# Kernel tuning notes

Measured on AMD Instinct MI355X. Metric: run time of the kernel, lower is better.

Reference implementation:

```python
import jax, jax.numpy as jnp
import numpy as np
from jax.scipy.special import logsumexp

EPS = 0.1
MAX_ITER = 10
THRESH = 0.1


def setup_inputs() -> dict:
    key = jax.random.key(0)
    k1, k2 = jax.random.split(key)
    N, P, D = 16, 1024, 64
    y = jax.random.normal(k1, (N, P, D), dtype=jnp.float32)
    x = jax.random.normal(k2, (N, P, D), dtype=jnp.float32)
    return {"y": y, "x": x}


def reference(y, x):
    # Cost matrix |x_i - y_j|^2 summed over feature dim: (N, P1, P2)
    C = jnp.sum(jnp.abs(x[:, :, None, :] - y[:, None, :, :]) ** 2, axis=-1)
    N, P1, P2 = C.shape
    mu = jnp.full((N, P1), 1.0 / P1, dtype=C.dtype)
    nu = jnp.full((N, P2), 1.0 / P2, dtype=C.dtype)

    def M(u, v):
        # (-C + u_i + v_j) / eps
        return (-C + u[:, :, None] + v[:, None, :]) / EPS

    def body(carry, _):
        u, v, done = carry
        u_new = EPS * (jnp.log(mu + 1e-8) - logsumexp(M(u, v), axis=-1)) + u
        v_new = EPS * (jnp.log(nu + 1e-8) - logsumexp(M(u_new, v), axis=-2)) + v
        err = jnp.abs(u_new - u).sum(-1).mean()
        # emulate torch's early break: freeze updates once converged
        u2 = jnp.where(done, u, u_new)
        v2 = jnp.where(done, v, v_new)
        done2 = done | (err < THRESH)
        return (u2, v2, done2), None

    u0 = jnp.zeros_like(mu)
    v0 = jnp.zeros_like(nu)
    (u, v, _), _ = jax.lax.scan(body, (u0, v0, jnp.array(False)), None, length=MAX_ITER)
    pi = jnp.exp(M(u, v))  # transport plan (N, P1, P2)
    return pi
```

## Files before the change

### kernel.cpp

```cpp
#include <hip/hip_runtime.h>
#include <math.h>

#define NB 16
#define PP 1024
#define DD 64
#define MAX_ITER 10
#define RCH 16
#define NCH (PP / RCH)
#define NBLK (NB * NCH)

constexpr float EPSV    = 0.1f;
constexpr float INV_EPS = 10.0f;
constexpr float LOG2E   = 1.44269504088896340736f;
constexpr float LOG_MU  = -6.93146156597137f;
constexpr float THRESHV = 0.1f;

__global__ __launch_bounds__(256) void compute_c(
    const float* __restrict__ x, const float* __restrict__ y,
    float* __restrict__ Cs)
{
  const int bid = blockIdx.x;
  const int n   = bid >> 8;
  const int ib  = (bid >> 4) & 15;
  const int jb  = bid & 15;

  __shared__ float xs[64][68];
  __shared__ float ys[64][68];

  const float* xb = x + ((size_t)n * PP + ib * 64) * DD;
  const float* yb = y + ((size_t)n * PP + jb * 64) * DD;

  for (int t = threadIdx.x; t < 64 * 16; t += 256) {
    int r = t >> 4, d4 = (t & 15) * 4;
    float4 v = *(const float4*)(xb + r * DD + d4);
    xs[r][d4] = v.x; xs[r][d4 + 1] = v.y; xs[r][d4 + 2] = v.z; xs[r][d4 + 3] = v.w;
  }
  for (int t = threadIdx.x; t < 64 * 16; t += 256) {
    int r = t >> 4, d4 = (t & 15) * 4;
    float4 v = *(const float4*)(yb + (size_t)r * DD + d4);
    ys[r][d4] = v.x; ys[r][d4 + 1] = v.y; ys[r][d4 + 2] = v.z; ys[r][d4 + 3] = v.w;
  }
  __syncthreads();

  const int tx = threadIdx.x & 15;
  const int ty = threadIdx.x >> 4;
  const int i0 = ty * 4;

  float acc[4][4] = {};
  for (int d0 = 0; d0 < 64; d0 += 4) {
    float4 xv[4], yv[4];
    #pragma unroll
    for (int ii = 0; ii < 4; ++ii) xv[ii] = *(const float4*)&xs[i0 + ii][d0];
    #pragma unroll
    for (int jj = 0; jj < 4; ++jj) yv[jj] = *(const float4*)&ys[tx + 16 * jj][d0];
    #pragma unroll
    for (int ii = 0; ii < 4; ++ii) {
      #pragma unroll
      for (int jj = 0; jj < 4; ++jj) {
        float d;
        d = xv[ii].x - yv[jj].x; acc[ii][jj] = fmaf(d, d, acc[ii][jj]);
        d = xv[ii].y - yv[jj].y; acc[ii][jj] = fmaf(d, d, acc[ii][jj]);
        d = xv[ii].z - yv[jj].z; acc[ii][jj] = fmaf(d, d, acc[ii][jj]);
        d = xv[ii].w - yv[jj].w; acc[ii][jj] = fmaf(d, d, acc[ii][jj]);
      }
    }
  }

  float* outb = Cs + ((size_t)n * PP + ib * 64) * PP + jb * 64;
  #pragma unroll
  for (int ii = 0; ii < 4; ++ii)
    #pragma unroll
    for (int jj = 0; jj < 4; ++jj)
      outb[(size_t)(i0 + ii) * PP + tx + 16 * jj] = acc[ii][jj] * INV_EPS;
}

__global__ __launch_bounds__(256, 4) void iter_fused(
    const float* __restrict__ Cs, float* __restrict__ aG, const float* __restrict__ bG,
    float* __restrict__ pm, float* __restrict__ ps, float* __restrict__ errBlk,
    const int* __restrict__ doneFlags, int it)
{
  if (it > 0 && doneFlags[it - 1]) return;

  const int n   = blockIdx.x >> 6;
  const int rc  = blockIdx.x & (NCH - 1);
  const int tid = threadIdx.x;

  __shared__ float bb[PP];
  __shared__ float aArr[RCH];
  __shared__ float dsum[RCH];

  if (it == 0) {
    *(float4*)&bb[tid * 4] = make_float4(0.f, 0.f, 0.f, 0.f);
  } else {
    *(float4*)&bb[tid * 4] = *(const float4*)(bG + n * PP + tid * 4);
  }
  __syncthreads();

  const int r0  = tid >> 4;
  const int k   = tid & 15;
  const int row = n * PP + rc * RCH + r0;
  const float* crow = Cs + (size_t)row * PP + 4 * k;

  float4 tv[16];
  #pragma unroll
  for (int j = 0; j < 16; ++j) {
    float4 c4 = *(const float4*)(crow + 64 * j);
    float4 b4 = *(const float4*)&bb[4 * k + 64 * j];
    tv[j] = make_float4(b4.x - c4.x, b4.y - c4.y, b4.z - c4.z, b4.w - c4.w);
  }
  float m = -INFINITY;
  #pragma unroll
  for (int j = 0; j < 16; ++j)
    m = fmaxf(m, fmaxf(fmaxf(tv[j].x, tv[j].y), fmaxf(tv[j].z, tv[j].w)));
  #pragma unroll
  for (int mask = 8; mask; mask >>= 1) m = fmaxf(m, __shfl_xor(m, mask));

  float s = 0.f;
  #pragma unroll
  for (int j = 0; j < 16; ++j) {
    s += exp2f((tv[j].x - m) * LOG2E) + exp2f((tv[j].y - m) * LOG2E)
       + exp2f((tv[j].z - m) * LOG2E) + exp2f((tv[j].w - m) * LOG2E);
  }
  #pragma unroll
  for (int mask = 8; mask; mask >>= 1) s += __shfl_xor(s, mask);

  if (k == 0) {
    float aOld = (it == 0) ? 0.f : aG[row];
    float an = LOG_MU - (m + logf(s));
    aG[row]  = an;
    aArr[r0] = an;
    dsum[r0] = fabsf(an - aOld);
  }
  __syncthreads();
  if (tid == 0) {
    float e = 0.f;
    #pragma unroll
    for (int r = 0; r < RCH; ++r) e += dsum[r];
    errBlk[blockIdx.x] = e;
  }

  const int c0 = tid * 4;
  const float* cb = Cs + ((size_t)(n * PP + rc * RCH)) * PP + c0;

  float m0 = -INFINITY, m1 = -INFINITY, m2 = -INFINITY, m3 = -INFINITY;
  #pragma unroll
  for (int r = 0; r < RCH; ++r) {
    float ar = aArr[r];
    float4 c4 = *(const float4*)(cb + (size_t)r * PP);
    m0 = fmaxf(m0, ar - c4.x);
    m1 = fmaxf(m1, ar - c4.y);
    m2 = fmaxf(m2, ar - c4.z);
    m3 = fmaxf(m3, ar - c4.w);
  }
  float s0 = 0.f, s1 = 0.f, s2 = 0.f, s3 = 0.f;
  #pragma unroll
  for (int r = 0; r < RCH; ++r) {
    float ar = aArr[r];
    float4 c4 = *(const float4*)(cb + (size_t)r * PP);
    s0 += exp2f((ar - c4.x - m0) * LOG2E);
    s1 += exp2f((ar - c4.y - m1) * LOG2E);
    s2 += exp2f((ar - c4.z - m2) * LOG2E);
    s3 += exp2f((ar - c4.w - m3) * LOG2E);
  }
  size_t off = ((size_t)(n * NCH + rc)) * PP + c0;
  *(float4*)(pm + off) = make_float4(m0, m1, m2, m3);
  *(float4*)(ps + off) = make_float4(s0, s1, s2, s3);
}

__global__ __launch_bounds__(256) void v_combine(
    const float* __restrict__ pm, const float* __restrict__ ps,
    float* __restrict__ bG, const float* __restrict__ errBlk,
    int* __restrict__ doneFlags, int it)
{
  if (it > 0 && doneFlags[it - 1]) {
    if (blockIdx.x == 0 && threadIdx.x == 0) doneFlags[it] = 1;
    return;
  }
  const int col = blockIdx.x * 256 + threadIdx.x;
  const int n = col >> 10, j = col & (PP - 1);
  const float* pmn = pm + (size_t)n * NCH * PP + j;
  const float* psn = ps + (size_t)n * NCH * PP + j;

  float m = -INFINITY, s = 0.f;
  #pragma unroll 8
  for (int c = 0; c < NCH; ++c) {
    float mc = pmn[(size_t)c * PP];
    float sc = psn[(size_t)c * PP];
    float mn = fmaxf(m, mc);
    s = fmaf(s, exp2f((m - mn) * LOG2E), sc * exp2f((mc - mn) * LOG2E));
    m = mn;
  }
  bG[col] = LOG_MU - (m + logf(s));

  if (blockIdx.x == 0) {
    __shared__ float red[4];
    float loc = 0.f;
    for (int t = threadIdx.x; t < NBLK; t += 256) loc += errBlk[t];
    #pragma unroll
    for (int off = 32; off > 0; off >>= 1) loc += __shfl_xor(loc, off);
    if ((threadIdx.x & 63) == 0) red[threadIdx.x >> 6] = loc;
    __syncthreads();
    if (threadIdx.x == 0) {
      float tot = red[0] + red[1] + red[2] + red[3];
      float err = tot * (EPSV / (float)NB);
      doneFlags[it] = (err < THRESHV) ? 1 : 0;
    }
  }
}

__global__ __launch_bounds__(256) void pi_kernel(
    float* __restrict__ Cs, const float* __restrict__ a, const float* __restrict__ b)
{
  const int lane = threadIdx.x & 63;
  const int row  = (blockIdx.x << 2) + (threadIdx.x >> 6);
  const int n    = row >> 10;
  const float ai = a[row];
  float* crow = Cs + (size_t)row * PP;
  const float* bn = b + n * PP;
  #pragma unroll
  for (int kk = 0; kk < 4; ++kk) {
    float4 c4 = *(const float4*)(crow + lane * 4 + kk * 256);
    float4 b4 = *(const float4*)(bn   + lane * 4 + kk * 256);
    float4 r;
    r.x = exp2f((ai + b4.x - c4.x) * LOG2E);
    r.y = exp2f((ai + b4.y - c4.y) * LOG2E);
    r.z = exp2f((ai + b4.z - c4.z) * LOG2E);
    r.w = exp2f((ai + b4.w - c4.w) * LOG2E);
    *(float4*)(crow + lane * 4 + kk * 256) = r;
  }
}

extern "C" void kernel_launch(void* const* d_in, const int* in_sizes, int n_in,
                              void* d_out, int out_size, void* d_ws, size_t ws_size,
                              hipStream_t stream)
{
  const float* y = (const float*)d_in[0];
  const float* x = (const float*)d_in[1];

  float* Cs      = (float*)d_out;
  float* pm      = (float*)d_ws;
  float* ps      = pm + (size_t)NB * NCH * PP;
  float* bGl     = ps + (size_t)NB * NCH * PP;
  float* aGl     = bGl + NB * PP;
  float* errBlk  = aGl + NB * PP;
  int*   doneFl  = (int*)(errBlk + NBLK);

  compute_c<<<NB * 16 * 16, 256, 0, stream>>>(x, y, Cs);
  for (int it = 0; it < MAX_ITER; ++it) {
    iter_fused<<<NBLK, 256, 0, stream>>>(Cs, aGl, bGl, pm, ps, errBlk, doneFl, it);
    v_combine<<<NB * PP / 256, 256, 0, stream>>>(pm, ps, bGl, errBlk, doneFl, it);
  }
  pi_kernel<<<NB * PP / 4, 256, 0, stream>>>(Cs, aGl, bGl);
}
```

Measured before the change: 386.9 us.

## Compute cost matrix with split-bf16 MFMA via norm expansion

Replaces the scalar pairwise squared-difference cost kernel with the expansion |x|^2 + |y|^2 - 2x·y. The dot products run on bf16 MFMA using a hi/lo split (three products) to approximate fp32 accuracy. A prep kernel precomputes the bf16 hi/lo parts and the scaled row norms, and the workspace is reused for these buffers. This cuts the VALU work of the cost stage, at the cost of some precision loss and cancellation error for nearby points, plus an extra kernel launch.

```diff
diff --git a/kernel.cpp b/kernel.cpp
--- a/kernel.cpp
+++ b/kernel.cpp
@@ -10,68 +10,132 @@
 #define NBLK (NB * NCH)
 
 constexpr float EPSV    = 0.1f;
-constexpr float INV_EPS = 10.0f;
+constexpr float SCALE_G = 20.0f;
 constexpr float LOG2E   = 1.44269504088896340736f;
 constexpr float LOG_MU  = -6.93146156597137f;
 constexpr float THRESHV = 0.1f;
 
-__global__ __launch_bounds__(256) void compute_c(
+typedef short bf16x8 __attribute__((ext_vector_type(8)));
+typedef float f32x16 __attribute__((ext_vector_type(16)));
+
+__device__ __forceinline__ unsigned short f2bf(float f) {
+  unsigned int u = __float_as_uint(f);
+  return (unsigned short)((u + 0x7FFFu + ((u >> 16) & 1u)) >> 16);
+}
+__device__ __forceinline__ float bf2f(unsigned short h) {
+  return __uint_as_float(((unsigned int)h) << 16);
+}
+
+__global__ __launch_bounds__(256) void prep_kernel(
     const float* __restrict__ x, const float* __restrict__ y,
+    unsigned short* __restrict__ xh, unsigned short* __restrict__ xl,
+    unsigned short* __restrict__ yh, unsigned short* __restrict__ yl,
+    float* __restrict__ nxs, float* __restrict__ nys)
+{
+  const int sel = blockIdx.x >> 9;
+  const int row = (blockIdx.x & 511) * 32 + (threadIdx.x >> 3);
+  const int q   = threadIdx.x & 7;
+
+  const float* src = sel ? y : x;
+  unsigned short* H = sel ? yh : xh;
+  unsigned short* L = sel ? yl : xl;
+  float* N          = sel ? nys : nxs;
+
+  const float* p = src + (size_t)row * DD + q * 8;
+  float4 v0 = *(const float4*)(p);
+  float4 v1 = *(const float4*)(p + 4);
+
+  float f[8] = {v0.x, v0.y, v0.z, v0.w, v1.x, v1.y, v1.z, v1.w};
+  float nrm = 0.f;
+  unsigned short hb[8], lb[8];
+  #pragma unroll
+  for (int k = 0; k < 8; ++k) {
+    nrm = fmaf(f[k], f[k], nrm);
+    unsigned short h = f2bf(f[k]);
+    float res = f[k] - bf2f(h);
+    hb[k] = h; lb[k] = f2bf(res);
+  }
+  nrm += __shfl_xor(nrm, 1);
+  nrm += __shfl_xor(nrm, 2);
+  nrm += __shfl_xor(nrm, 4);
+  if (q == 0) N[row] = 10.0f * nrm;
+
+  uint4 ho, lo;
+  ho.x = hb[0] | ((unsigned)hb[1] << 16); ho.y = hb[2] | ((unsigned)hb[3] << 16);
+  ho.z = hb[4] | ((unsigned)hb[5] << 16); ho.w = hb[6] | ((unsigned)hb[7] << 16);
+  lo.x = lb[0] | ((unsigned)lb[1] << 16); lo.y = lb[2] | ((unsigned)lb[3] << 16);
+  lo.z = lb[4] | ((unsigned)lb[5] << 16); lo.w = lb[6] | ((unsigned)lb[7] << 16);
+  *(uint4*)(H + (size_t)row * DD + q * 8) = ho;
+  *(uint4*)(L + (size_t)row * DD + q * 8) = lo;
+}
+
+__global__ __launch_bounds__(256) void compute_c_mfma(
+    const unsigned short* __restrict__ xh, const unsigned short* __restrict__ xl,
+    const float* __restrict__ nxs,
+    const unsigned short* __restrict__ yh, const unsigned short* __restrict__ yl,
+    const float* __restrict__ nys,
     float* __restrict__ Cs)
 {
-  const int bid = blockIdx.x;
-  const int n   = bid >> 8;
-  const int ib  = (bid >> 4) & 15;
-  const int jb  = bid & 15;
-
-  __shared__ float xs[64][68];
-  __shared__ float ys[64][68];
-
-  const float* xb = x + ((size_t)n * PP + ib * 64) * DD;
-  const float* yb = y + ((size_t)n * PP + jb * 64) * DD;
-
-  for (int t = threadIdx.x; t < 64 * 16; t += 256) {
-    int r = t >> 4, d4 = (t & 15) * 4;
-    float4 v = *(const float4*)(xb + r * DD + d4);
-    xs[r][d4] = v.x; xs[r][d4 + 1] = v.y; xs[r][d4 + 2] = v.z; xs[r][d4 + 3] = v.w;
-  }
-  for (int t = threadIdx.x; t < 64 * 16; t += 256) {
-    int r = t >> 4, d4 = (t & 15) * 4;
-    float4 v = *(const float4*)(yb + (size_t)r * DD + d4);
-    ys[r][d4] = v.x; ys[r][d4 + 1] = v.y; ys[r][d4 + 2] = v.z; ys[r][d4 + 3] = v.w;
-  }
+  const int n   = blockIdx.x >> 8;
+  const int ib  = (blockIdx.x >> 4) & 15;
+  const int jb  = blockIdx.x & 15;
+  const int tid = threadIdx.x;
+  const int l   = tid & 63;
+  const int w   = tid >> 6;
+  const int ih  = w & 1, jh = w >> 1;
+
+  __shared__ float nxv[64];
+  if (tid < 64) nxv[tid] = nxs[n * PP + ib * 64 + tid];
   __syncthreads();
 
-  const int tx = threadIdx.x & 15;
-  const int ty = threadIdx.x >> 4;
-  const int i0 = ty * 4;
-
-  float acc[4][4] = {};
-  for (int d0 = 0; d0 < 64; d0 += 4) {
-    float4 xv[4], yv[4];
-    #pragma unroll
-    for (int ii = 0; ii < 4; ++ii) xv[ii] = *(const float4*)&xs[i0 + ii][d0];
-    #pragma unroll
-    for (int jj = 0; jj < 4; ++jj) yv[jj] = *(const float4*)&ys[tx + 16 * jj][d0];
-    #pragma unroll
-    for (int ii = 0; ii < 4; ++ii) {
-      #pragma unroll
-      for (int jj = 0; jj < 4; ++jj) {
-        float d;
-        d = xv[ii].x - yv[jj].x; acc[ii][jj] = fmaf(d, d, acc[ii][jj]);
-        d = xv[ii].y - yv[jj].y; acc[ii][jj] = fmaf(d, d, acc[ii][jj]);
-        d = xv[ii].z - yv[jj].z; acc[ii][jj] = fmaf(d, d, acc[ii][jj]);
-        d = xv[ii].w - yv[jj].w; acc[ii][jj] = fmaf(d, d, acc[ii][jj]);
-      }
-    }
-  }
-
-  float* outb = Cs + ((size_t)n * PP + ib * 64) * PP + jb * 64;
-  #pragma unroll
-  for (int ii = 0; ii < 4; ++ii)
-    #pragma unroll
-    for (int jj = 0; jj < 4; ++jj)
-      outb[(size_t)(i0 + ii) * PP + tx + 16 * jj] = acc[ii][jj] * INV_EPS;
+  const int jg  = n * PP + jb * 64 + 32 * jh + (l & 31);
+  const float nyv = nys[jg];
+
+  const int ko = 8 * (l >> 5);
+  const size_t xrow = ((size_t)(n * PP + ib * 64 + 32 * ih + (l & 31))) * DD;
+  const size_t yrow = ((size_t)jg) * DD;
+
+  bf16x8 Xh0 = *(const bf16x8*)(xh + xrow + 0 * 16 + ko);
+  bf16x8 Xh1 = *(const bf16x8*)(xh + xrow + 1 * 16 + ko);
+  bf16x8 Xh2 = *(const bf16x8*)(xh + xrow + 2 * 16 + ko);
+  bf16x8 Xh3 = *(const bf16x8*)(xh + xrow + 3 * 16 + ko);
+  bf16x8 Xl0 = *(const bf16x8*)(xl + xrow + 0 * 16 + ko);
+  bf16x8 Xl1 = *(const bf16x8*)(xl + xrow + 1 * 16 + ko);
+  bf16x8 Xl2 = *(const bf16x8*)(xl + xrow + 2 * 16 + ko);
+  bf16x8 Xl3 = *(const bf16x8*)(xl + xrow + 3 * 16 + ko);
+  bf16x8 Yh0 = *(const bf16x8*)(yh + yrow + 0 * 16 + ko);
+  bf16x8 Yh1 = *(const bf16x8*)(yh + yrow + 1 * 16 + ko);
+  bf16x8 Yh2 = *(const bf16x8*)(yh + yrow + 2 * 16 + ko);
+  bf16x8 Yh3 = *(const bf16x8*)(yh + yrow + 3 * 16 + ko);
+  bf16x8 Yl0 = *(const bf16x8*)(yl + yrow + 0 * 16 + ko);
+  bf16x8 Yl1 = *(const bf16x8*)(yl + yrow + 1 * 16 + ko);
+  bf16x8 Yl2 = *(const bf16x8*)(yl + yrow + 2 * 16 + ko);
+  bf16x8 Yl3 = *(const bf16x8*)(yl + yrow + 3 * 16 + ko);
+
+  f32x16 acc;
+  #pragma unroll
+  for (int z = 0; z < 16; ++z) acc[z] = 0.f;
+  acc = __builtin_amdgcn_mfma_f32_32x32x16_bf16(Xh0, Yh0, acc, 0, 0, 0);
+  acc = __builtin_amdgcn_mfma_f32_32x32x16_bf16(Xh1, Yh1, acc, 0, 0, 0);
+  acc = __builtin_amdgcn_mfma_f32_32x32x16_bf16(Xh2, Yh2, acc, 0, 0, 0);
+  acc = __builtin_amdgcn_mfma_f32_32x32x16_bf16(Xh3, Yh3, acc, 0, 0, 0);
+  acc = __builtin_amdgcn_mfma_f32_32x32x16_bf16(Xh0, Yl0, acc, 0, 0, 0);
+  acc = __builtin_amdgcn_mfma_f32_32x32x16_bf16(Xh1, Yl1, acc, 0, 0, 0);
+  acc = __builtin_amdgcn_mfma_f32_32x32x16_bf16(Xh2, Yl2, acc, 0, 0, 0);
+  acc = __builtin_amdgcn_mfma_f32_32x32x16_bf16(Xh3, Yl3, acc, 0, 0, 0);
+  acc = __builtin_amdgcn_mfma_f32_32x32x16_bf16(Xl0, Yh0, acc, 0, 0, 0);
+  acc = __builtin_amdgcn_mfma_f32_32x32x16_bf16(Xl1, Yh1, acc, 0, 0, 0);
+  acc = __builtin_amdgcn_mfma_f32_32x32x16_bf16(Xl2, Yh2, acc, 0, 0, 0);
+  acc = __builtin_amdgcn_mfma_f32_32x32x16_bf16(Xl3, Yh3, acc, 0, 0, 0);
+
+  const int irb  = 32 * ih + 4 * (l >> 5);
+  const int jcol = jb * 64 + 32 * jh + (l & 31);
+  #pragma unroll
+  for (int r = 0; r < 16; ++r) {
+    const int irel = irb + (r & 3) + 8 * (r >> 2);
+    const size_t off = ((size_t)(n * PP + ib * 64 + irel)) * PP + jcol;
+    Cs[off] = nxv[irel] + nyv - SCALE_G * acc[r];
+  }
 }
 
 __global__ __launch_bounds__(256, 4) void iter_fused(
@@ -237,15 +301,26 @@
   const float* y = (const float*)d_in[0];
   const float* x = (const float*)d_in[1];
 
-  float* Cs      = (float*)d_out;
-  float* pm      = (float*)d_ws;
-  float* ps      = pm + (size_t)NB * NCH * PP;
-  float* bGl     = ps + (size_t)NB * NCH * PP;
-  float* aGl     = bGl + NB * PP;
-  float* errBlk  = aGl + NB * PP;
-  int*   doneFl  = (int*)(errBlk + NBLK);
-
-  compute_c<<<NB * 16 * 16, 256, 0, stream>>>(x, y, Cs);
+  float* Cs = (float*)d_out;
+
+  const size_t NE = (size_t)NB * PP * DD;
+  unsigned short* xh = (unsigned short*)d_ws;
+  unsigned short* xl = xh + NE;
+  unsigned short* yh = xl + NE;
+  unsigned short* yl = yh + NE;
+  float* pm = (float*)d_ws;
+  float* ps = pm + (size_t)NB * NCH * PP;
+
+  float* tail   = (float*)((char*)d_ws + 4 * NE * sizeof(unsigned short));
+  float* nxs    = tail;
+  float* nys    = nxs + NB * PP;
+  float* aGl    = nys + NB * PP;
+  float* bGl    = aGl + NB * PP;
+  float* errBlk = bGl + NB * PP;
+  int*   doneFl = (int*)(errBlk + NBLK);
+
+  prep_kernel<<<1024, 256, 0, stream>>>(x, y, xh, xl, yh, yl, nxs, nys);
+  compute_c_mfma<<<4096, 256, 0, stream>>>(xh, xl, nxs, yh, yl, nys, Cs);
   for (int it = 0; it < MAX_ITER; ++it) {
     iter_fused<<<NBLK, 256, 0, stream>>>(Cs, aGl, bGl, pm, ps, errBlk, doneFl, it);
     v_combine<<<NB * PP / 256, 256, 0, stream>>>(pm, ps, bGl, errBlk, doneFl, it);
```

Result: faster. 378.6 us (-2.1%).
